# Kernel tuning notes

Measured on AMD Instinct MI355X. Metric: run time of the kernel, lower is better.

The kernel has to match this reference:

```python
import jax, jax.numpy as jnp
import numpy as np

HID = 256
SLOTS = 64
K = 2
TAU = 8.0
EPS = 1e-5


def setup_inputs() -> dict:
    key = jax.random.key(0)
    ks = jax.random.split(key, 8)
    B, T = 512, 256
    s = lambda fan_in: 1.0 / np.sqrt(fan_in)
    return {
        "x": jax.random.uniform(ks[0], (B, T, 1), jnp.float32, 0.0, 10.0),
        "W_embed": jax.random.uniform(ks[1], (HID, 1), jnp.float32, -1.0, 1.0),
        "b_embed": jax.random.uniform(ks[2], (HID,), jnp.float32, -1.0, 1.0),
        "W_update": jax.random.uniform(ks[3], (HID, HID), jnp.float32, -s(HID), s(HID)),
        "b_update": jax.random.uniform(ks[4], (HID,), jnp.float32, -s(HID), s(HID)),
        "gamma": jnp.ones((HID,), jnp.float32),
        "beta": jnp.zeros((HID,), jnp.float32),
        "W_out": jax.random.uniform(ks[5], (10, HID), jnp.float32, -s(HID), s(HID)),
        "b_out": jax.random.uniform(ks[6], (10,), jnp.float32, -s(HID), s(HID)),
        "context_strength": jnp.float32(0.2),
    }


def _gaussian_attention(pointer, num_positions):
    # pointer: [B] float. Returns indices [B,5] int32, weights [B,5] float.
    offsets = jnp.arange(-K, K + 1)
    base = jnp.clip(jnp.floor(pointer).astype(jnp.int32), 0, num_positions - 1)
    indices = (base[:, None] + offsets[None, :]) % num_positions
    delta = indices.astype(pointer.dtype) - pointer[:, None]
    weights = jax.nn.softmax(-(delta ** 2) / TAU, axis=1)
    return indices, weights


def reference(x, W_embed, b_embed, W_update, b_update, gamma, beta, W_out, b_out, context_strength):
    B, T, _ = x.shape
    cs = jax.nn.sigmoid(context_strength)

    def step(carry, x_t):
        h, memory, pointer = carry  # [B,H], [B,SLOTS,H], [B]
        inp = jnp.tanh(x_t @ W_embed.T + b_embed)           # [B,H]
        indices, weights = _gaussian_attention(pointer, SLOTS)
        neighborhood = jnp.take_along_axis(memory, indices[:, :, None], axis=1)  # [B,5,H]
        context = jnp.einsum('bk,bkh->bh', weights, neighborhood)
        combined = inp + cs * context
        h = jnp.tanh((combined + h) @ W_update.T + b_update)
        mu = jnp.mean(h, axis=-1, keepdims=True)
        var = jnp.mean((h - mu) ** 2, axis=-1, keepdims=True)
        h = (h - mu) * jax.lax.rsqrt(var + EPS) * gamma + beta
        contribution = weights[:, :, None] * h[:, None, :]   # [B,5,H]
        memory = jax.vmap(lambda m, i, c: m.at[i].add(c))(memory, indices, contribution)
        pointer = (pointer + 1.0) % SLOTS
        return (h, memory, pointer), None

    h0 = jnp.zeros((B, HID), x.dtype)
    mem0 = jnp.zeros((B, SLOTS, HID), x.dtype)
    ptr0 = jnp.zeros((B,), x.dtype)
    (h, _, _), _ = jax.lax.scan(step, (h0, mem0, ptr0), jnp.swapaxes(x, 0, 1))
    return h @ W_out.T + b_out
```

## Files before the change

### kernel.cpp

```cpp
#include <hip/hip_runtime.h>


#define TT 256

typedef __bf16 bf16x8 __attribute__((ext_vector_type(8)));
typedef float  f32x4  __attribute__((ext_vector_type(4)));

__device__ __forceinline__ float fast_tanh(float x) {
    float e = __expf(2.f * x);
    return 1.f - __fdividef(2.f, e + 1.f);
}

template<int CTRL, int RM>
__device__ __forceinline__ float dpp_add(float v) {
    int t = __builtin_amdgcn_update_dpp(0, __float_as_int(v), CTRL, RM, 0xf, true);
    return v + __int_as_float(t);
}
__device__ __forceinline__ float wave_sum63(float v) {
    v = dpp_add<0xB1,  0xf>(v);
    v = dpp_add<0x4E,  0xf>(v);
    v = dpp_add<0x141, 0xf>(v);
    v = dpp_add<0x140, 0xf>(v);
    v = dpp_add<0x142, 0xa>(v);
    v = dpp_add<0x143, 0xc>(v);
    return v;
}

#define SMEM_BYTES 138416

__global__ __launch_bounds__(512, 2)
void postnorm_kernel(const float* __restrict__ x,
                     const float* __restrict__ W_embed,
                     const float* __restrict__ b_embed,
                     const float* __restrict__ W_update,
                     const float* __restrict__ b_update,
                     const float* __restrict__ gamma,
                     const float* __restrict__ beta,
                     const float* __restrict__ W_out,
                     const float* __restrict__ b_out,
                     const float* __restrict__ ctx_s,
                     float* __restrict__ out)
{
    extern __shared__ __align__(16) char smem[];
    float*  s_mem  = (float*)(smem);
    float*  s_x    = (float*)(smem + 131072);
    float*  s_y    = (float*)(smem + 133120);
    __bf16* s_v    = (__bf16*)(smem + 135168);
    float*  s_red1 = (float*)(smem + 136224);
    float*  s_red2 = (float*)(smem + 136256);
    float*  s_wt   = (float*)(smem + 136288);
    float*  s_oacc = (float*)(smem + 138336);

    const int tid  = threadIdx.x;
    const int n    = tid >> 8;
    const int i    = tid & 255;
    const int wave = tid >> 6;
    const int lane = tid & 63;
    const int bn   = lane & 15;
    const int quad = lane >> 4;
    const int r0   = blockIdx.x * 2;

    {   f32x4 z = {0.f, 0.f, 0.f, 0.f};
        f32x4* p = (f32x4*)s_mem;
        #pragma unroll
        for (int k = 0; k < 16; ++k) p[tid + k * 512] = z;
    }
    if (tid < 264) ((unsigned int*)s_v)[tid] = 0u;
    s_x[tid] = x[(r0 + n) * TT + i];
    if (tid < 20) s_oacc[tid] = 0.f;

    if (tid < 64) {
        float wv[5]; float ssum = 0.f;
        #pragma unroll
        for (int k = 0; k < 5; ++k) {
            int idx = (tid + k - 2) & 63;
            float d = (float)idx - (float)tid;
            wv[k] = expf(-(d * d) * 0.125f);
            ssum += wv[k];
        }
        #pragma unroll
        for (int k = 0; k < 5; ++k) s_wt[tid * 8 + k] = wv[k] / ssum;
    }

    const float we  = W_embed[i];
    const float be  = b_embed[i];
    const float bu  = b_update[i];
    const float gm  = gamma[i];
    const float btt = beta[i];
    const float csv = 1.f / (1.f + expf(-ctx_s[0]));

    bf16x8 wfa[2][8];
    #pragma unroll
    for (int mt = 0; mt < 2; ++mt) {
        #pragma unroll
        for (int kt = 0; kt < 8; ++kt) {
            const float* wp = W_update + (wave * 32 + mt * 16 + bn) * 256
                                       + kt * 32 + quad * 8;
            f32x4 a = *(const f32x4*)wp;
            f32x4 b = *(const f32x4*)(wp + 4);
            bf16x8 f;
            f[0] = (__bf16)a[0]; f[1] = (__bf16)a[1];
            f[2] = (__bf16)a[2]; f[3] = (__bf16)a[3];
            f[4] = (__bf16)b[0]; f[5] = (__bf16)b[1];
            f[6] = (__bf16)b[2]; f[7] = (__bf16)b[3];
            wfa[mt][kt] = f;
        }
    }

    __syncthreads();
    {
        float inp = fast_tanh(s_x[n * 256] * we + be);
        s_v[n * 264 + i] = (__bf16)inp;
    }

    float wt0, wt1, wt2, wt3, wt4;
    {   f32x4 wv = *(const f32x4*)(s_wt);
        wt0 = wv[0]; wt1 = wv[1]; wt2 = wv[2]; wt3 = wv[3]; wt4 = s_wt[4];
    }
    __syncthreads();

    float hn = 0.f;
    float w0 = 0.f, w1 = 0.f, w2 = 0.f, w3 = 0.f, w4 = 0.f;
    float* mcol = s_mem + (n << 14) + i;
    const __bf16* vsrc = s_v + (bn & 1) * 264 + quad * 8;

    #pragma unroll 1
    for (int t = 0; t < TT; ++t) {
        f32x4 a0a = {0,0,0,0}, a0b = {0,0,0,0}, a1a = {0,0,0,0}, a1b = {0,0,0,0};
        #pragma unroll
        for (int kt = 0; kt < 4; ++kt) {
            bf16x8 bfr0 = *(const bf16x8*)(vsrc + kt * 32);
            bf16x8 bfr1 = *(const bf16x8*)(vsrc + (kt + 4) * 32);
            a0a = __builtin_amdgcn_mfma_f32_16x16x32_bf16(wfa[0][kt],     bfr0, a0a, 0, 0, 0);
            a1a = __builtin_amdgcn_mfma_f32_16x16x32_bf16(wfa[1][kt],     bfr0, a1a, 0, 0, 0);
            a0b = __builtin_amdgcn_mfma_f32_16x16x32_bf16(wfa[0][kt + 4], bfr1, a0b, 0, 0, 0);
            a1b = __builtin_amdgcn_mfma_f32_16x16x32_bf16(wfa[1][kt + 4], bfr1, a1b, 0, 0, 0);
        }
        if (bn < 2) {
            f32x4 y0 = a0a + a0b, y1 = a1a + a1b;
            float* yb = s_y + bn * 256 + wave * 32 + quad * 4;
            *(f32x4*)yb        = y0;
            *(f32x4*)(yb + 16) = y1;
        }
        __syncthreads();

        float yt = fast_tanh(s_y[tid] + bu);
        float s1 = wave_sum63(yt);
        float s2 = wave_sum63(yt * yt);
        if (lane == 63) { s_red1[wave] = s1; s_red2[wave] = s2; }
        __syncthreads();

        f32x4 r1 = *(const f32x4*)(s_red1 + n * 4);
        f32x4 r2 = *(const f32x4*)(s_red2 + n * 4);
        float S1 = (r1[0] + r1[1]) + (r1[2] + r1[3]);
        float S2 = (r2[0] + r2[1]) + (r2[2] + r2[3]);
        float mu   = S1 * (1.f / 256.f);
        float var  = S2 * (1.f / 256.f) - mu * mu;
        float rstd = rsqrtf(var + 1e-5f);
        hn = (yt - mu) * rstd * gm + btt;

        w0 += wt0 * hn; w1 += wt1 * hn; w2 += wt2 * hn;
        w3 += wt3 * hn; w4 += wt4 * hn;

        if (t < TT - 1) {
            mcol[((t - 2) & 63) << 8] = w0;
            float nf = mcol[((t + 3) & 63) << 8];
            w0 = w1; w1 = w2; w2 = w3; w3 = w4; w4 = nf;
            f32x4 nw = *(const f32x4*)(s_wt + ((t + 1) & 63) * 8);
            float nw4 = s_wt[((t + 1) & 63) * 8 + 4];
            float ctx = ((nw[0] * w0 + nw[1] * w1) + (nw[2] * w2 + nw[3] * w3))
                      + nw4 * w4;
            float inp = fast_tanh(s_x[n * 256 + t + 1] * we + be);
            float v = inp + csv * ctx + hn;
            s_v[n * 264 + i] = (__bf16)v;
            wt0 = nw[0]; wt1 = nw[1]; wt2 = nw[2]; wt3 = nw[3]; wt4 = nw4;
        }
        __syncthreads();
    }

    #pragma unroll
    for (int o = 0; o < 10; ++o) {
        float p = hn * W_out[o * 256 + i];
        #pragma unroll
        for (int m = 32; m >= 1; m >>= 1) p += __shfl_xor(p, m, 64);
        if (lane == 0) atomicAdd(&s_oacc[n * 10 + o], p);
    }
    __syncthreads();
    if (tid < 20) {
        int nn = tid / 10, o = tid % 10;
        out[(r0 + nn) * 10 + o] = s_oacc[tid] + b_out[o];
    }
}

extern "C" void kernel_launch(void* const* d_in, const int* in_sizes, int n_in,
                              void* d_out, int out_size, void* d_ws, size_t ws_size,
                              hipStream_t stream) {
    const float* x    = (const float*)d_in[0];
    const float* W_e  = (const float*)d_in[1];
    const float* b_e  = (const float*)d_in[2];
    const float* W_u  = (const float*)d_in[3];
    const float* b_u  = (const float*)d_in[4];
    const float* gmm  = (const float*)d_in[5];
    const float* bta  = (const float*)d_in[6];
    const float* W_o  = (const float*)d_in[7];
    const float* b_o  = (const float*)d_in[8];
    const float* cst  = (const float*)d_in[9];
    float* out = (float*)d_out;

    (void)hipFuncSetAttribute(reinterpret_cast<const void*>(postnorm_kernel),
                              hipFuncAttributeMaxDynamicSharedMemorySize,
                              SMEM_BYTES);

    postnorm_kernel<<<dim3(256), dim3(512), SMEM_BYTES, stream>>>(
        x, W_e, b_e, W_u, b_u, gmm, bta, W_o, b_o, cst, out);
}
```

Measured before the change: 319.8 us.

## Process one batch row per block with 256 threads and prefetch next-step loads

Each block now handles a single batch row with 256 threads (4 waves) instead of two rows with 512 threads, and the grid doubles to 512 blocks. Each wave now holds 64 output rows of W_update in registers (4x8 bf16 fragments), so it issues 32 MFMAs per step, all sharing one B-operand load. Smaller LDS per block allows more resident blocks and shortens barriers. The memory, weight and x loads for the next step are moved to the top of the loop so their latency overlaps the MFMA work. The cost is more register pressure from the doubled weight fragments and fewer waves sharing each step's serial latency.

```diff
diff --git a/kernel.cpp b/kernel.cpp
--- a/kernel.cpp
+++ b/kernel.cpp
@@ -26,9 +26,9 @@
     return v;
 }
 
-#define SMEM_BYTES 138416
-
-__global__ __launch_bounds__(512, 2)
+#define SMEM_BYTES 70224
+
+__global__ __launch_bounds__(256, 2)
 void postnorm_kernel(const float* __restrict__ x,
                      const float* __restrict__ W_embed,
                      const float* __restrict__ b_embed,
@@ -43,31 +43,28 @@
 {
     extern __shared__ __align__(16) char smem[];
     float*  s_mem  = (float*)(smem);
-    float*  s_x    = (float*)(smem + 131072);
-    float*  s_y    = (float*)(smem + 133120);
-    __bf16* s_v    = (__bf16*)(smem + 135168);
-    float*  s_red1 = (float*)(smem + 136224);
-    float*  s_red2 = (float*)(smem + 136256);
-    float*  s_wt   = (float*)(smem + 136288);
-    float*  s_oacc = (float*)(smem + 138336);
+    float*  s_x    = (float*)(smem + 65536);
+    float*  s_y    = (float*)(smem + 66560);
+    __bf16* s_v    = (__bf16*)(smem + 67584);
+    float*  s_red1 = (float*)(smem + 68096);
+    float*  s_red2 = (float*)(smem + 68112);
+    float*  s_wt   = (float*)(smem + 68128);
+    float*  s_oacc = (float*)(smem + 70176);
 
     const int tid  = threadIdx.x;
-    const int n    = tid >> 8;
-    const int i    = tid & 255;
     const int wave = tid >> 6;
     const int lane = tid & 63;
     const int bn   = lane & 15;
     const int quad = lane >> 4;
-    const int r0   = blockIdx.x * 2;
+    const int r    = blockIdx.x;
 
     {   f32x4 z = {0.f, 0.f, 0.f, 0.f};
         f32x4* p = (f32x4*)s_mem;
         #pragma unroll
-        for (int k = 0; k < 16; ++k) p[tid + k * 512] = z;
-    }
-    if (tid < 264) ((unsigned int*)s_v)[tid] = 0u;
-    s_x[tid] = x[(r0 + n) * TT + i];
-    if (tid < 20) s_oacc[tid] = 0.f;
+        for (int k = 0; k < 16; ++k) p[tid + k * 256] = z;
+    }
+    s_x[tid] = x[r * TT + tid];
+    if (tid < 10) s_oacc[tid] = 0.f;
 
     if (tid < 64) {
         float wv[5]; float ssum = 0.f;
@@ -82,19 +79,19 @@
         for (int k = 0; k < 5; ++k) s_wt[tid * 8 + k] = wv[k] / ssum;
     }
 
-    const float we  = W_embed[i];
-    const float be  = b_embed[i];
-    const float bu  = b_update[i];
-    const float gm  = gamma[i];
-    const float btt = beta[i];
+    const float we  = W_embed[tid];
+    const float be  = b_embed[tid];
+    const float bu  = b_update[tid];
+    const float gm  = gamma[tid];
+    const float btt = beta[tid];
     const float csv = 1.f / (1.f + expf(-ctx_s[0]));
 
-    bf16x8 wfa[2][8];
+    bf16x8 wfa[4][8];
     #pragma unroll
-    for (int mt = 0; mt < 2; ++mt) {
+    for (int mt = 0; mt < 4; ++mt) {
         #pragma unroll
         for (int kt = 0; kt < 8; ++kt) {
-            const float* wp = W_update + (wave * 32 + mt * 16 + bn) * 256
+            const float* wp = W_update + (wave * 64 + mt * 16 + bn) * 256
                                        + kt * 32 + quad * 8;
             f32x4 a = *(const f32x4*)wp;
             f32x4 b = *(const f32x4*)(wp + 4);
@@ -109,8 +106,8 @@
 
     __syncthreads();
     {
-        float inp = fast_tanh(s_x[n * 256] * we + be);
-        s_v[n * 264 + i] = (__bf16)inp;
+        float inp = fast_tanh(s_x[0] * we + be);
+        s_v[tid] = (__bf16)inp;
     }
 
     float wt0, wt1, wt2, wt3, wt4;
@@ -121,26 +118,31 @@
 
     float hn = 0.f;
     float w0 = 0.f, w1 = 0.f, w2 = 0.f, w3 = 0.f, w4 = 0.f;
-    float* mcol = s_mem + (n << 14) + i;
-    const __bf16* vsrc = s_v + (bn & 1) * 264 + quad * 8;
+    float* mcol = s_mem + tid;
+    const __bf16* vsrc = s_v + quad * 8;
 
     #pragma unroll 1
     for (int t = 0; t < TT; ++t) {
-        f32x4 a0a = {0,0,0,0}, a0b = {0,0,0,0}, a1a = {0,0,0,0}, a1b = {0,0,0,0};
-        #pragma unroll
-        for (int kt = 0; kt < 4; ++kt) {
-            bf16x8 bfr0 = *(const bf16x8*)(vsrc + kt * 32);
-            bf16x8 bfr1 = *(const bf16x8*)(vsrc + (kt + 4) * 32);
-            a0a = __builtin_amdgcn_mfma_f32_16x16x32_bf16(wfa[0][kt],     bfr0, a0a, 0, 0, 0);
-            a1a = __builtin_amdgcn_mfma_f32_16x16x32_bf16(wfa[1][kt],     bfr0, a1a, 0, 0, 0);
-            a0b = __builtin_amdgcn_mfma_f32_16x16x32_bf16(wfa[0][kt + 4], bfr1, a0b, 0, 0, 0);
-            a1b = __builtin_amdgcn_mfma_f32_16x16x32_bf16(wfa[1][kt + 4], bfr1, a1b, 0, 0, 0);
-        }
-        if (bn < 2) {
-            f32x4 y0 = a0a + a0b, y1 = a1a + a1b;
-            float* yb = s_y + bn * 256 + wave * 32 + quad * 4;
-            *(f32x4*)yb        = y0;
-            *(f32x4*)(yb + 16) = y1;
+        float nf  = mcol[((t + 3) & 63) << 8];
+        f32x4 nw  = *(const f32x4*)(s_wt + ((t + 1) & 63) * 8);
+        float nw4 = s_wt[((t + 1) & 63) * 8 + 4];
+        float xn  = s_x[(t + 1) & 255];
+
+        f32x4 a0 = {0,0,0,0}, a1 = {0,0,0,0}, a2 = {0,0,0,0}, a3 = {0,0,0,0};
+        #pragma unroll
+        for (int kt = 0; kt < 8; ++kt) {
+            bf16x8 bfr = *(const bf16x8*)(vsrc + kt * 32);
+            a0 = __builtin_amdgcn_mfma_f32_16x16x32_bf16(wfa[0][kt], bfr, a0, 0, 0, 0);
+            a1 = __builtin_amdgcn_mfma_f32_16x16x32_bf16(wfa[1][kt], bfr, a1, 0, 0, 0);
+            a2 = __builtin_amdgcn_mfma_f32_16x16x32_bf16(wfa[2][kt], bfr, a2, 0, 0, 0);
+            a3 = __builtin_amdgcn_mfma_f32_16x16x32_bf16(wfa[3][kt], bfr, a3, 0, 0, 0);
+        }
+        if (bn == 0) {
+            float* yb = s_y + wave * 64 + quad * 4;
+            *(f32x4*)yb        = a0;
+            *(f32x4*)(yb + 16) = a1;
+            *(f32x4*)(yb + 32) = a2;
+            *(f32x4*)(yb + 48) = a3;
         }
         __syncthreads();
 
@@ -150,8 +152,8 @@
         if (lane == 63) { s_red1[wave] = s1; s_red2[wave] = s2; }
         __syncthreads();
 
-        f32x4 r1 = *(const f32x4*)(s_red1 + n * 4);
-        f32x4 r2 = *(const f32x4*)(s_red2 + n * 4);
+        f32x4 r1 = *(const f32x4*)s_red1;
+        f32x4 r2 = *(const f32x4*)s_red2;
         float S1 = (r1[0] + r1[1]) + (r1[2] + r1[3]);
         float S2 = (r2[0] + r2[1]) + (r2[2] + r2[3]);
         float mu   = S1 * (1.f / 256.f);
@@ -164,15 +166,12 @@
 
         if (t < TT - 1) {
             mcol[((t - 2) & 63) << 8] = w0;
-            float nf = mcol[((t + 3) & 63) << 8];
             w0 = w1; w1 = w2; w2 = w3; w3 = w4; w4 = nf;
-            f32x4 nw = *(const f32x4*)(s_wt + ((t + 1) & 63) * 8);
-            float nw4 = s_wt[((t + 1) & 63) * 8 + 4];
             float ctx = ((nw[0] * w0 + nw[1] * w1) + (nw[2] * w2 + nw[3] * w3))
                       + nw4 * w4;
-            float inp = fast_tanh(s_x[n * 256 + t + 1] * we + be);
+            float inp = fast_tanh(xn * we + be);
             float v = inp + csv * ctx + hn;
-            s_v[n * 264 + i] = (__bf16)v;
+            s_v[tid] = (__bf16)v;
             wt0 = nw[0]; wt1 = nw[1]; wt2 = nw[2]; wt3 = nw[3]; wt4 = nw4;
         }
         __syncthreads();
@@ -180,15 +179,14 @@
 
     #pragma unroll
     for (int o = 0; o < 10; ++o) {
-        float p = hn * W_out[o * 256 + i];
+        float p = hn * W_out[o * 256 + tid];
         #pragma unroll
         for (int m = 32; m >= 1; m >>= 1) p += __shfl_xor(p, m, 64);
-        if (lane == 0) atomicAdd(&s_oacc[n * 10 + o], p);
+        if (lane == 0) atomicAdd(&s_oacc[o], p);
     }
     __syncthreads();
-    if (tid < 20) {
-        int nn = tid / 10, o = tid % 10;
-        out[(r0 + nn) * 10 + o] = s_oacc[tid] + b_out[o];
+    if (tid < 10) {
+        out[r * 10 + tid] = s_oacc[tid] + b_out[tid];
     }
 }
 
@@ -211,6 +209,6 @@
                               hipFuncAttributeMaxDynamicSharedMemorySize,
                               SMEM_BYTES);
 
-    postnorm_kernel<<<dim3(256), dim3(512), SMEM_BYTES, stream>>>(
+    postnorm_kernel<<<dim3(512), dim3(256), SMEM_BYTES, stream>>>(
         x, W_e, b_e, W_u, b_u, gmm, bta, W_o, b_o, cst, out);
 }
```

Result: slower. 360.1 us (+12.6%).
